# Performance work log

Measured on AMD Instinct MI355X. Metric: run time of the kernel, lower is better.

The kernel has to match this reference:

```python
import jax, jax.numpy as jnp
import numpy as np

NUM_LAYERS = 2
MAG = 5 / 10.0  # magnitude=5 on a 0-10 scale
FILL = 0.5      # gray fill for out-of-bounds pixels (images in [0,1])
ENH = 1.0 + 0.9 * MAG  # enhancement factor magnitude (brightness/contrast/sharpness)


def _bilinear(img, xi, yi):
    H, W, _ = img.shape
    x0 = jnp.floor(xi); y0 = jnp.floor(yi)
    wx = xi - x0; wy = yi - y0
    def gather(yy, xx):
        valid = (xx >= 0) & (xx <= W - 1) & (yy >= 0) & (yy <= H - 1)
        v = img[jnp.clip(yy, 0, H - 1).astype(jnp.int32),
                jnp.clip(xx, 0, W - 1).astype(jnp.int32)]
        return jnp.where(valid[..., None], v, FILL)
    return (gather(y0, x0) * ((1 - wx) * (1 - wy))[..., None]
            + gather(y0, x0 + 1) * (wx * (1 - wy))[..., None]
            + gather(y0 + 1, x0) * ((1 - wx) * wy)[..., None]
            + gather(y0 + 1, x0 + 1) * (wx * wy)[..., None])


def _affine(img, a, b, tx, c, d, ty):
    # inverse affine map about image center, bilinear resample
    H, W, _ = img.shape
    ys, xs = jnp.meshgrid(jnp.arange(H, dtype=jnp.float32),
                          jnp.arange(W, dtype=jnp.float32), indexing='ij')
    cx = (W - 1) * 0.5; cy = (H - 1) * 0.5
    xi = a * (xs - cx) + b * (ys - cy) + tx + cx
    yi = c * (xs - cx) + d * (ys - cy) + ty + cy
    return _bilinear(img, xi, yi)


def _blend(a, b, f):
    return jnp.clip(a + f * (b - a), 0.0, 1.0)


def _smooth(img):
    # 3x3 smoothing kernel used by PIL/TF sharpness
    k = jnp.array([[1., 1., 1.], [1., 5., 1.], [1., 1., 1.]], jnp.float32) / 13.0
    H, W, _ = img.shape
    p = jnp.pad(img, ((1, 1), (1, 1), (0, 0)), mode='edge')
    out = jnp.zeros_like(img)
    for i in range(3):
        for j in range(3):
            out = out + k[i, j] * p[i:i + H, j:j + W]
    return out


def _rotate(img, s):
    th = s * (30.0 * MAG) * (np.pi / 180.0)
    co, si = jnp.cos(th), jnp.sin(th)
    return _affine(img, co, si, 0.0, -si, co, 0.0)

def _shear_x(img, s):
    sh = s * 0.3 * MAG
    return _affine(img, 1.0, -sh, 0.0, 0.0, 1.0, 0.0)

def _shear_y(img, s):
    sh = s * 0.3 * MAG
    return _affine(img, 1.0, 0.0, 0.0, -sh, 1.0, 0.0)

def _trans_x(img, s):
    t = s * 0.3 * MAG * img.shape[1]
    return _affine(img, 1.0, 0.0, -t, 0.0, 1.0, 0.0)

def _trans_y(img, s):
    t = s * 0.3 * MAG * img.shape[0]
    return _affine(img, 1.0, 0.0, 0.0, 0.0, 1.0, -t)

def _brightness(img, s):
    f = jnp.where(s > 0, ENH, 1.0 / ENH)
    return _blend(jnp.zeros_like(img), img, f)

def _contrast(img, s):
    f = jnp.where(s > 0, ENH, 1.0 / ENH)
    return _blend(jnp.mean(img) * jnp.ones_like(img), img, f)

def _sharpness(img, s):
    f = jnp.where(s > 0, ENH, 1.0 / ENH)
    return _blend(_smooth(img), img, f)


BRANCHES = [_rotate, _shear_x, _shear_y, _trans_x, _trans_y,
            _brightness, _contrast, _sharpness]


def _apply_one(img, ops, signs):
    # img: [H,W,3]; ops, signs: [NUM_LAYERS]
    for l in range(NUM_LAYERS):
        s = (2 * signs[l] - 1).astype(jnp.float32)
        img = jax.lax.switch(ops[l], BRANCHES, img, s)
    return img


def setup_inputs() -> dict:
    key = jax.random.key(0)
    k1, k2, k3 = jax.random.split(key, 3)
    B, H, W = 64, 512, 512
    images = jax.random.uniform(k1, (B, H, W, 3), dtype=jnp.float32)
    op_ids = jax.random.randint(k2, (B, NUM_LAYERS), 0, len(BRANCHES), dtype=jnp.int32)
    signs = jax.random.randint(k3, (B, NUM_LAYERS), 0, 2, dtype=jnp.int32)
    return {"images": images, "op_ids": op_ids, "signs": signs}


def reference(images, op_ids, signs):
    return jax.vmap(_apply_one)(images, op_ids, signs)
```

## Files before the change

kernel.cpp:

```cpp
#include <hip/hip_runtime.h>
#include <math.h>

#define IMH 512
#define IMW 512
#define NIMG 64
#define NPIX (IMH*IMW)
#define NELEM (NPIX*3)
#define CXF 255.5f
#define CYF 255.5f
#define ENHF 1.45f
#define INVENHF (1.0f/1.45f)
#define FILLF 0.5f
#define MBPI 64
#define TW 64
#define TH 16
#define MAXLDS 2560

struct F3 { float x, y, z; };

__device__ __forceinline__ F3 mk3(float v){ F3 r; r.x=v; r.y=v; r.z=v; return r; }

__device__ __forceinline__ F3 ldpix(const float* __restrict__ im, int y, int x){
  const float* p = im + (y*IMW + x)*3;
  F3 r; r.x=p[0]; r.y=p[1]; r.z=p[2]; return r;
}

__device__ __forceinline__ F3 clip01(F3 v){
  F3 r;
  r.x = fminf(fmaxf(v.x, 0.f), 1.f);
  r.y = fminf(fmaxf(v.y, 0.f), 1.f);
  r.z = fminf(fmaxf(v.z, 0.f), 1.f);
  return r;
}

__device__ __forceinline__ void affine_params(int op, float s,
    float& a, float& b, float& tx, float& c, float& d, float& ty){
  a = 1.f; b = 0.f; tx = 0.f; c = 0.f; d = 1.f; ty = 0.f;
  if (op == 0){
    a = 0.96592582628907f; b = s * 0.25881904510252f; c = -b; d = a;
  } else if (op == 1){
    b = -s * 0.15f;
  } else if (op == 2){
    c = -s * 0.15f;
  } else if (op == 3){
    tx = -s * 76.8f;
  } else if (op == 4){
    ty = -s * 76.8f;
  }
}

__device__ __forceinline__ F3 bilin_img(const float* __restrict__ im, float xi, float yi){
  float x0 = floorf(xi), y0 = floorf(yi);
  float wx = xi - x0, wy = yi - y0;
  F3 acc = mk3(0.f);
  #pragma unroll
  for (int cidx = 0; cidx < 4; cidx++){
    int dx = cidx & 1, dy = cidx >> 1;
    float xx = x0 + (float)dx, yy = y0 + (float)dy;
    float w = (dx ? wx : (1.f - wx)) * (dy ? wy : (1.f - wy));
    F3 v;
    if (xx >= 0.f && xx <= (float)(IMW-1) && yy >= 0.f && yy <= (float)(IMH-1))
      v = ldpix(im, (int)yy, (int)xx);
    else
      v = mk3(FILLF);
    acc.x += w * v.x; acc.y += w * v.y; acc.z += w * v.z;
  }
  return acc;
}

__device__ F3 eval0(const float* __restrict__ im, int op, float s, float mean0, int x, int y){
  if (op < 5){
    float a,b,tx,c,d,ty; affine_params(op, s, a, b, tx, c, d, ty);
    float fx = (float)x - CXF, fy = (float)y - CYF;
    return bilin_img(im, a*fx + b*fy + tx + CXF, c*fx + d*fy + ty + CYF);
  }
  F3 v = ldpix(im, y, x);
  float f = (s > 0.f) ? ENHF : INVENHF;
  if (op == 5){
    F3 r; r.x = f*v.x; r.y = f*v.y; r.z = f*v.z; return clip01(r);
  }
  if (op == 6){
    F3 r;
    r.x = mean0 + f*(v.x - mean0);
    r.y = mean0 + f*(v.y - mean0);
    r.z = mean0 + f*(v.z - mean0);
    return clip01(r);
  }
  F3 sm; sm.x = (5.f/13.f)*v.x; sm.y = (5.f/13.f)*v.y; sm.z = (5.f/13.f)*v.z;
  #pragma unroll
  for (int dy = -1; dy <= 1; dy++){
    #pragma unroll
    for (int dx = -1; dx <= 1; dx++){
      if (dx == 0 && dy == 0) continue;
      int yy = min(max(y + dy, 0), IMH-1);
      int xx = min(max(x + dx, 0), IMW-1);
      F3 q = ldpix(im, yy, xx);
      sm.x += (1.f/13.f)*q.x; sm.y += (1.f/13.f)*q.y; sm.z += (1.f/13.f)*q.z;
    }
  }
  F3 r;
  r.x = sm.x + f*(v.x - sm.x);
  r.y = sm.y + f*(v.y - sm.y);
  r.z = sm.z + f*(v.z - sm.z);
  return clip01(r);
}

__device__ __forceinline__ float block_reduce(float v){
  #pragma unroll
  for (int off = 32; off > 0; off >>= 1) v += __shfl_down(v, off, 64);
  __shared__ float sm[4];
  int lane = threadIdx.x & 63, wid = threadIdx.x >> 6;
  if (lane == 0) sm[wid] = v;
  __syncthreads();
  float r = 0.f;
  if (threadIdx.x == 0) r = sm[0] + sm[1] + sm[2] + sm[3];
  return r;
}

__global__ __launch_bounds__(256) void mean0_kernel(const float* __restrict__ images,
    const int* __restrict__ ops, float* __restrict__ means){
  int img = blockIdx.x / MBPI;
  if (ops[2*img] != 6) return;
  const float* im = images + (size_t)img * NELEM;
  float s = 0.f;
  for (int i = (blockIdx.x % MBPI)*256 + threadIdx.x; i < NELEM; i += MBPI*256)
    s += im[i];
  s = block_reduce(s);
  if (threadIdx.x == 0) atomicAdd(&means[2*img], s * (1.0f/(float)NELEM));
}

__global__ __launch_bounds__(256) void mean1_kernel(const float* __restrict__ images,
    const int* __restrict__ ops, const int* __restrict__ signs, float* __restrict__ means){
  int img = blockIdx.x / MBPI;
  if (ops[2*img + 1] != 6) return;
  int op0 = ops[2*img];
  float s0 = signs[2*img] ? 1.f : -1.f;
  float mean0 = means[2*img];
  const float* im = images + (size_t)img * NELEM;
  float s = 0.f;
  for (int p = (blockIdx.x % MBPI)*256 + threadIdx.x; p < NPIX; p += MBPI*256){
    F3 v = eval0(im, op0, s0, mean0, p & (IMW-1), p >> 9);
    s += v.x + v.y + v.z;
  }
  s = block_reduce(s);
  if (threadIdx.x == 0) atomicAdd(&means[2*img + 1], s * (1.0f/(float)NELEM));
}

__global__ __launch_bounds__(256) void apply_kernel(const float* __restrict__ images,
    const int* __restrict__ ops, const int* __restrict__ signs,
    const float* __restrict__ means, float* __restrict__ out){
  int img  = blockIdx.x >> 8;
  int tile = blockIdx.x & 255;
  int tx0 = (tile & 7) * TW;
  int ty0 = (tile >> 3) * TH;
  const float* im = images + (size_t)img * NELEM;
  int op0 = ops[2*img], op1 = ops[2*img + 1];
  float s0 = signs[2*img]     ? 1.f : -1.f;
  float s1 = signs[2*img + 1] ? 1.f : -1.f;
  float mean0 = means[2*img], mean1 = means[2*img + 1];

  float a1=1.f,b1=0.f,txx=0.f,c1=0.f,d1=1.f,tyy=0.f;
  int bx0, by0, bx1, by1;
  if (op1 < 5){
    affine_params(op1, s1, a1, b1, txx, c1, d1, tyy);
    float xmin = 1e30f, xmax = -1e30f, ymin = 1e30f, ymax = -1e30f;
    #pragma unroll
    for (int i = 0; i < 4; i++){
      float fx = (float)(tx0 + (i & 1) * (TW - 1)) - CXF;
      float fy = (float)(ty0 + (i >> 1) * (TH - 1)) - CYF;
      float xi = a1*fx + b1*fy + txx + CXF;
      float yi = c1*fx + d1*fy + tyy + CYF;
      xmin = fminf(xmin, xi); xmax = fmaxf(xmax, xi);
      ymin = fminf(ymin, yi); ymax = fmaxf(ymax, yi);
    }
    bx0 = (int)floorf(xmin) - 1; bx1 = (int)floorf(xmax) + 2;
    by0 = (int)floorf(ymin) - 1; by1 = (int)floorf(ymax) + 2;
  } else if (op1 == 7){
    bx0 = tx0 - 1; bx1 = tx0 + TW; by0 = ty0 - 1; by1 = ty0 + TH;
  } else {
    bx0 = tx0; bx1 = tx0 + TW - 1; by0 = ty0; by1 = ty0 + TH - 1;
  }
  bx0 = max(bx0, 0); by0 = max(by0, 0);
  bx1 = min(bx1, IMW - 1); by1 = min(by1, IMH - 1);
  int bw = bx1 - bx0 + 1, bh = by1 - by0 + 1;
  int nstage = (bw > 0 && bh > 0) ? bw * bh : 0;

  __shared__ float lds[MAXLDS * 3];
  for (int idx = threadIdx.x; idx < nstage; idx += 256){
    int iy = idx / bw;
    int ix = idx - iy * bw;
    F3 v = eval0(im, op0, s0, mean0, bx0 + ix, by0 + iy);
    lds[idx*3 + 0] = v.x; lds[idx*3 + 1] = v.y; lds[idx*3 + 2] = v.z;
  }
  __syncthreads();

  int row = threadIdx.x >> 4;
  int xbase = tx0 + ((threadIdx.x & 15) << 2);
  int y = ty0 + row;
  float f1 = (s1 > 0.f) ? ENHF : INVENHF;
  F3 res[4];
  #pragma unroll
  for (int q = 0; q < 4; q++){
    int x = xbase + q;
    F3 o;
    if (op1 < 5){
      float fx = (float)x - CXF, fy = (float)y - CYF;
      float xi = a1*fx + b1*fy + txx + CXF;
      float yi = c1*fx + d1*fy + tyy + CYF;
      float xf0 = floorf(xi), yf0 = floorf(yi);
      float wx = xi - xf0, wy = yi - yf0;
      o = mk3(0.f);
      #pragma unroll
      for (int ci = 0; ci < 4; ci++){
        int dx = ci & 1, dy = ci >> 1;
        float xx = xf0 + (float)dx, yy = yf0 + (float)dy;
        float w = (dx ? wx : (1.f - wx)) * (dy ? wy : (1.f - wy));
        F3 v;
        if (xx >= 0.f && xx <= (float)(IMW-1) && yy >= 0.f && yy <= (float)(IMH-1)){
          int li = (((int)yy - by0) * bw + ((int)xx - bx0)) * 3;
          v.x = lds[li]; v.y = lds[li+1]; v.z = lds[li+2];
        } else v = mk3(FILLF);
        o.x += w * v.x; o.y += w * v.y; o.z += w * v.z;
      }
    } else {
      int li0 = ((y - by0) * bw + (x - bx0)) * 3;
      F3 v; v.x = lds[li0]; v.y = lds[li0+1]; v.z = lds[li0+2];
      if (op1 == 5){
        o.x = f1*v.x; o.y = f1*v.y; o.z = f1*v.z;
        o = clip01(o);
      } else if (op1 == 6){
        o.x = mean1 + f1*(v.x - mean1);
        o.y = mean1 + f1*(v.y - mean1);
        o.z = mean1 + f1*(v.z - mean1);
        o = clip01(o);
      } else {
        F3 sm; sm.x = (5.f/13.f)*v.x; sm.y = (5.f/13.f)*v.y; sm.z = (5.f/13.f)*v.z;
        #pragma unroll
        for (int dy = -1; dy <= 1; dy++){
          #pragma unroll
          for (int dx = -1; dx <= 1; dx++){
            if (dx == 0 && dy == 0) continue;
            int yy = min(max(y + dy, 0), IMH-1);
            int xx = min(max(x + dx, 0), IMW-1);
            int li = ((yy - by0) * bw + (xx - bx0)) * 3;
            sm.x += (1.f/13.f)*lds[li];
            sm.y += (1.f/13.f)*lds[li+1];
            sm.z += (1.f/13.f)*lds[li+2];
          }
        }
        o.x = sm.x + f1*(v.x - sm.x);
        o.y = sm.y + f1*(v.y - sm.y);
        o.z = sm.z + f1*(v.z - sm.z);
        o = clip01(o);
      }
    }
    res[q] = o;
  }

  float4 o0 = make_float4(res[0].x, res[0].y, res[0].z, res[1].x);
  float4 o1 = make_float4(res[1].y, res[1].z, res[2].x, res[2].y);
  float4 o2 = make_float4(res[2].z, res[3].x, res[3].y, res[3].z);
  float4* op = (float4*)(out + ((size_t)img * NPIX + (size_t)y * IMW + xbase) * 3);
  op[0] = o0; op[1] = o1; op[2] = o2;
}

extern "C" void kernel_launch(void* const* d_in, const int* in_sizes, int n_in,
                              void* d_out, int out_size, void* d_ws, size_t ws_size,
                              hipStream_t stream){
  const float* images = (const float*)d_in[0];
  const int*   ops    = (const int*)d_in[1];
  const int*   signs  = (const int*)d_in[2];
  float* out   = (float*)d_out;
  float* means = (float*)d_ws;

  hipMemsetAsync(means, 0, 2*NIMG*sizeof(float), stream);
  mean0_kernel<<<NIMG*MBPI, 256, 0, stream>>>(images, ops, means);
  mean1_kernel<<<NIMG*MBPI, 256, 0, stream>>>(images, ops, signs, means);
  apply_kernel<<<NIMG*256, 256, 0, stream>>>(images, ops, signs, means, out);
}
```

Before: 496.1 us.

## Square tiles, direct path for pointwise ops, fast-path bilinear, vectorized mean

The apply tile changes from 64x16 to 32x32, which lowers LDS halo usage for rotated or sheared footprints. When the second op is brightness or contrast, the kernel evaluates op0 directly per pixel and skips LDS staging and the barrier. Bilinear sampling gets an interior fast path that reads the 2x2 neighbours with fewer bounds checks. The mean kernels now read with float4 loads, and mean1 uses more blocks per image to spread its work. In exchange there are more atomics in mean1, and the staging footprint differs for affine ops.

```diff
diff --git a/kernel.cpp b/kernel.cpp
--- a/kernel.cpp
+++ b/kernel.cpp
@@ -11,10 +11,11 @@
 #define ENHF 1.45f
 #define INVENHF (1.0f/1.45f)
 #define FILLF 0.5f
-#define MBPI 64
-#define TW 64
-#define TH 16
-#define MAXLDS 2560
+#define MBPI0 64
+#define MBPI1 512
+#define TW 32
+#define TH 32
+#define MAXLDS 1800
 
 struct F3 { float x, y, z; };
 
@@ -50,22 +51,34 @@
 }
 
 __device__ __forceinline__ F3 bilin_img(const float* __restrict__ im, float xi, float yi){
-  float x0 = floorf(xi), y0 = floorf(yi);
-  float wx = xi - x0, wy = yi - y0;
-  F3 acc = mk3(0.f);
-  #pragma unroll
-  for (int cidx = 0; cidx < 4; cidx++){
-    int dx = cidx & 1, dy = cidx >> 1;
-    float xx = x0 + (float)dx, yy = y0 + (float)dy;
-    float w = (dx ? wx : (1.f - wx)) * (dy ? wy : (1.f - wy));
-    F3 v;
-    if (xx >= 0.f && xx <= (float)(IMW-1) && yy >= 0.f && yy <= (float)(IMH-1))
-      v = ldpix(im, (int)yy, (int)xx);
-    else
-      v = mk3(FILLF);
-    acc.x += w * v.x; acc.y += w * v.y; acc.z += w * v.z;
-  }
-  return acc;
+  float x0f = floorf(xi), y0f = floorf(yi);
+  float wx = xi - x0f, wy = yi - y0f;
+  float w00 = (1.f-wx)*(1.f-wy), w01 = wx*(1.f-wy);
+  float w10 = (1.f-wx)*wy,       w11 = wx*wy;
+  int x0 = (int)x0f, y0 = (int)y0f;
+  F3 r;
+  if (x0 >= 0 && y0 >= 0 && x0 < IMW-1 && y0 < IMH-1){
+    const float* p0 = im + (y0*IMW + x0)*3;
+    const float* p1 = p0 + IMW*3;
+    r.x = w00*p0[0] + w01*p0[3] + w10*p1[0] + w11*p1[3];
+    r.y = w00*p0[1] + w01*p0[4] + w10*p1[1] + w11*p1[4];
+    r.z = w00*p0[2] + w01*p0[5] + w10*p1[2] + w11*p1[5];
+  } else {
+    r = mk3(0.f);
+    #pragma unroll
+    for (int cidx = 0; cidx < 4; cidx++){
+      int dx = cidx & 1, dy = cidx >> 1;
+      int xx = x0 + dx, yy = y0 + dy;
+      float w = (dx ? wx : (1.f - wx)) * (dy ? wy : (1.f - wy));
+      F3 v;
+      if (xx >= 0 && xx < IMW && yy >= 0 && yy < IMH)
+        v = ldpix(im, yy, xx);
+      else
+        v = mk3(FILLF);
+      r.x += w * v.x; r.y += w * v.y; r.z += w * v.z;
+    }
+  }
+  return r;
 }
 
 __device__ F3 eval0(const float* __restrict__ im, int op, float s, float mean0, int x, int y){
@@ -119,31 +132,42 @@
 
 __global__ __launch_bounds__(256) void mean0_kernel(const float* __restrict__ images,
     const int* __restrict__ ops, float* __restrict__ means){
-  int img = blockIdx.x / MBPI;
+  int img = blockIdx.x / MBPI0;
   if (ops[2*img] != 6) return;
-  const float* im = images + (size_t)img * NELEM;
+  const float4* im = (const float4*)(images + (size_t)img * NELEM);
   float s = 0.f;
-  for (int i = (blockIdx.x % MBPI)*256 + threadIdx.x; i < NELEM; i += MBPI*256)
-    s += im[i];
+  for (int i = (blockIdx.x % MBPI0)*256 + threadIdx.x; i < NELEM/4; i += MBPI0*256){
+    float4 v = im[i];
+    s += v.x + v.y + v.z + v.w;
+  }
   s = block_reduce(s);
   if (threadIdx.x == 0) atomicAdd(&means[2*img], s * (1.0f/(float)NELEM));
 }
 
 __global__ __launch_bounds__(256) void mean1_kernel(const float* __restrict__ images,
     const int* __restrict__ ops, const int* __restrict__ signs, float* __restrict__ means){
-  int img = blockIdx.x / MBPI;
+  int img = blockIdx.x / MBPI1;
   if (ops[2*img + 1] != 6) return;
   int op0 = ops[2*img];
   float s0 = signs[2*img] ? 1.f : -1.f;
   float mean0 = means[2*img];
   const float* im = images + (size_t)img * NELEM;
   float s = 0.f;
-  for (int p = (blockIdx.x % MBPI)*256 + threadIdx.x; p < NPIX; p += MBPI*256){
+  for (int p = (blockIdx.x % MBPI1)*256 + threadIdx.x; p < NPIX; p += MBPI1*256){
     F3 v = eval0(im, op0, s0, mean0, p & (IMW-1), p >> 9);
     s += v.x + v.y + v.z;
   }
   s = block_reduce(s);
   if (threadIdx.x == 0) atomicAdd(&means[2*img + 1], s * (1.0f/(float)NELEM));
+}
+
+__device__ __forceinline__ void store4(float* __restrict__ out, int img, int y, int xbase,
+                                       const F3* res){
+  float4 o0 = make_float4(res[0].x, res[0].y, res[0].z, res[1].x);
+  float4 o1 = make_float4(res[1].y, res[1].z, res[2].x, res[2].y);
+  float4 o2 = make_float4(res[2].z, res[3].x, res[3].y, res[3].z);
+  float4* op = (float4*)(out + ((size_t)img * NPIX + (size_t)y * IMW + xbase) * 3);
+  op[0] = o0; op[1] = o1; op[2] = o2;
 }
 
 __global__ __launch_bounds__(256) void apply_kernel(const float* __restrict__ images,
@@ -151,13 +175,37 @@
     const float* __restrict__ means, float* __restrict__ out){
   int img  = blockIdx.x >> 8;
   int tile = blockIdx.x & 255;
-  int tx0 = (tile & 7) * TW;
-  int ty0 = (tile >> 3) * TH;
+  int tx0 = (tile & 15) * TW;
+  int ty0 = (tile >> 4) * TH;
   const float* im = images + (size_t)img * NELEM;
   int op0 = ops[2*img], op1 = ops[2*img + 1];
   float s0 = signs[2*img]     ? 1.f : -1.f;
   float s1 = signs[2*img + 1] ? 1.f : -1.f;
   float mean0 = means[2*img], mean1 = means[2*img + 1];
+
+  int row   = threadIdx.x >> 3;
+  int xbase = tx0 + ((threadIdx.x & 7) << 2);
+  int y     = ty0 + row;
+  float f1 = (s1 > 0.f) ? ENHF : INVENHF;
+
+  if (op1 == 5 || op1 == 6){
+    F3 res[4];
+    #pragma unroll
+    for (int q = 0; q < 4; q++){
+      F3 v = eval0(im, op0, s0, mean0, xbase + q, y);
+      F3 o;
+      if (op1 == 5){
+        o.x = f1*v.x; o.y = f1*v.y; o.z = f1*v.z;
+      } else {
+        o.x = mean1 + f1*(v.x - mean1);
+        o.y = mean1 + f1*(v.y - mean1);
+        o.z = mean1 + f1*(v.z - mean1);
+      }
+      res[q] = clip01(o);
+    }
+    store4(out, img, y, xbase, res);
+    return;
+  }
 
   float a1=1.f,b1=0.f,txx=0.f,c1=0.f,d1=1.f,tyy=0.f;
   int bx0, by0, bx1, by1;
@@ -175,10 +223,8 @@
     }
     bx0 = (int)floorf(xmin) - 1; bx1 = (int)floorf(xmax) + 2;
     by0 = (int)floorf(ymin) - 1; by1 = (int)floorf(ymax) + 2;
-  } else if (op1 == 7){
+  } else {
     bx0 = tx0 - 1; bx1 = tx0 + TW; by0 = ty0 - 1; by1 = ty0 + TH;
-  } else {
-    bx0 = tx0; bx1 = tx0 + TW - 1; by0 = ty0; by1 = ty0 + TH - 1;
   }
   bx0 = max(bx0, 0); by0 = max(by0, 0);
   bx1 = min(bx1, IMW - 1); by1 = min(by1, IMH - 1);
@@ -194,10 +240,6 @@
   }
   __syncthreads();
 
-  int row = threadIdx.x >> 4;
-  int xbase = tx0 + ((threadIdx.x & 15) << 2);
-  int y = ty0 + row;
-  float f1 = (s1 > 0.f) ? ENHF : INVENHF;
   F3 res[4];
   #pragma unroll
   for (int q = 0; q < 4; q++){
@@ -209,59 +251,55 @@
       float yi = c1*fx + d1*fy + tyy + CYF;
       float xf0 = floorf(xi), yf0 = floorf(yi);
       float wx = xi - xf0, wy = yi - yf0;
-      o = mk3(0.f);
-      #pragma unroll
-      for (int ci = 0; ci < 4; ci++){
-        int dx = ci & 1, dy = ci >> 1;
-        float xx = xf0 + (float)dx, yy = yf0 + (float)dy;
-        float w = (dx ? wx : (1.f - wx)) * (dy ? wy : (1.f - wy));
-        F3 v;
-        if (xx >= 0.f && xx <= (float)(IMW-1) && yy >= 0.f && yy <= (float)(IMH-1)){
-          int li = (((int)yy - by0) * bw + ((int)xx - bx0)) * 3;
-          v.x = lds[li]; v.y = lds[li+1]; v.z = lds[li+2];
-        } else v = mk3(FILLF);
-        o.x += w * v.x; o.y += w * v.y; o.z += w * v.z;
+      float w00 = (1.f-wx)*(1.f-wy), w01 = wx*(1.f-wy);
+      float w10 = (1.f-wx)*wy,       w11 = wx*wy;
+      int x0 = (int)xf0, y0 = (int)yf0;
+      if (x0 >= 0 && y0 >= 0 && x0 < IMW-1 && y0 < IMH-1){
+        const float* q0 = lds + ((y0 - by0) * bw + (x0 - bx0)) * 3;
+        const float* q1 = q0 + bw * 3;
+        o.x = w00*q0[0] + w01*q0[3] + w10*q1[0] + w11*q1[3];
+        o.y = w00*q0[1] + w01*q0[4] + w10*q1[1] + w11*q1[4];
+        o.z = w00*q0[2] + w01*q0[5] + w10*q1[2] + w11*q1[5];
+      } else {
+        o = mk3(0.f);
+        #pragma unroll
+        for (int ci = 0; ci < 4; ci++){
+          int dx = ci & 1, dy = ci >> 1;
+          int xx = x0 + dx, yy = y0 + dy;
+          float w = (dx ? wx : (1.f - wx)) * (dy ? wy : (1.f - wy));
+          F3 v;
+          if (xx >= 0 && xx < IMW && yy >= 0 && yy < IMH){
+            int li = ((yy - by0) * bw + (xx - bx0)) * 3;
+            v.x = lds[li]; v.y = lds[li+1]; v.z = lds[li+2];
+          } else v = mk3(FILLF);
+          o.x += w * v.x; o.y += w * v.y; o.z += w * v.z;
+        }
       }
     } else {
       int li0 = ((y - by0) * bw + (x - bx0)) * 3;
       F3 v; v.x = lds[li0]; v.y = lds[li0+1]; v.z = lds[li0+2];
-      if (op1 == 5){
-        o.x = f1*v.x; o.y = f1*v.y; o.z = f1*v.z;
-        o = clip01(o);
-      } else if (op1 == 6){
-        o.x = mean1 + f1*(v.x - mean1);
-        o.y = mean1 + f1*(v.y - mean1);
-        o.z = mean1 + f1*(v.z - mean1);
-        o = clip01(o);
-      } else {
-        F3 sm; sm.x = (5.f/13.f)*v.x; sm.y = (5.f/13.f)*v.y; sm.z = (5.f/13.f)*v.z;
+      F3 sm; sm.x = (5.f/13.f)*v.x; sm.y = (5.f/13.f)*v.y; sm.z = (5.f/13.f)*v.z;
+      #pragma unroll
+      for (int dy = -1; dy <= 1; dy++){
         #pragma unroll
-        for (int dy = -1; dy <= 1; dy++){
-          #pragma unroll
-          for (int dx = -1; dx <= 1; dx++){
-            if (dx == 0 && dy == 0) continue;
-            int yy = min(max(y + dy, 0), IMH-1);
-            int xx = min(max(x + dx, 0), IMW-1);
-            int li = ((yy - by0) * bw + (xx - bx0)) * 3;
-            sm.x += (1.f/13.f)*lds[li];
-            sm.y += (1.f/13.f)*lds[li+1];
-            sm.z += (1.f/13.f)*lds[li+2];
-          }
+        for (int dx = -1; dx <= 1; dx++){
+          if (dx == 0 && dy == 0) continue;
+          int yy = min(max(y + dy, 0), IMH-1);
+          int xx = min(max(x + dx, 0), IMW-1);
+          int li = ((yy - by0) * bw + (xx - bx0)) * 3;
+          sm.x += (1.f/13.f)*lds[li];
+          sm.y += (1.f/13.f)*lds[li+1];
+          sm.z += (1.f/13.f)*lds[li+2];
         }
-        o.x = sm.x + f1*(v.x - sm.x);
-        o.y = sm.y + f1*(v.y - sm.y);
-        o.z = sm.z + f1*(v.z - sm.z);
-        o = clip01(o);
       }
-    }
-    res[q] = o;
-  }
-
-  float4 o0 = make_float4(res[0].x, res[0].y, res[0].z, res[1].x);
-  float4 o1 = make_float4(res[1].y, res[1].z, res[2].x, res[2].y);
-  float4 o2 = make_float4(res[2].z, res[3].x, res[3].y, res[3].z);
-  float4* op = (float4*)(out + ((size_t)img * NPIX + (size_t)y * IMW + xbase) * 3);
-  op[0] = o0; op[1] = o1; op[2] = o2;
+      o.x = sm.x + f1*(v.x - sm.x);
+      o.y = sm.y + f1*(v.y - sm.y);
+      o.z = sm.z + f1*(v.z - sm.z);
+    }
+    res[q] = clip01(o);
+  }
+
+  store4(out, img, y, xbase, res);
 }
 
 extern "C" void kernel_launch(void* const* d_in, const int* in_sizes, int n_in,
@@ -274,7 +312,7 @@
   float* means = (float*)d_ws;
 
   hipMemsetAsync(means, 0, 2*NIMG*sizeof(float), stream);
-  mean0_kernel<<<NIMG*MBPI, 256, 0, stream>>>(images, ops, means);
-  mean1_kernel<<<NIMG*MBPI, 256, 0, stream>>>(images, ops, signs, means);
+  mean0_kernel<<<NIMG*MBPI0, 256, 0, stream>>>(images, ops, means);
+  mean1_kernel<<<NIMG*MBPI1, 256, 0, stream>>>(images, ops, signs, means);
   apply_kernel<<<NIMG*256, 256, 0, stream>>>(images, ops, signs, means, out);
 }
```

After: 424.8 us. 14.4% less time.
